# Kernel optimization log

Hardware: AMD Instinct MI355X
Metric: run time of the kernel (lower is better)

The kernel has to match this reference:

```python
import jax, jax.numpy as jnp
import numpy as np

B, N, NH = 16, 2048, 64
DROP = 0.1


def setup_inputs() -> dict:
    key = jax.random.key(0)
    ks = jax.random.split(key, 10)
    s = 1.0 / np.sqrt(NH)
    return {
        "adj": jax.random.normal(ks[0], (B, N, N), jnp.float32) * 0.02,
        "diff": jax.random.normal(ks[1], (B, N, N), jnp.float32) * 0.02,
        "sub_local_pos1": jax.random.normal(ks[2], (B, N, NH), jnp.float32),
        "sub_local_pos2": jax.random.normal(ks[3], (B, N, NH), jnp.float32),
        "sub_local_neg1": jax.random.normal(ks[4], (B, N, NH), jnp.float32),
        "sub_local_neg2": jax.random.normal(ks[5], (B, N, NH), jnp.float32),
        # Bilinear params: weight [1, NH, NH], bias [1] (xavier-ish scale)
        "W0": jax.random.normal(ks[6], (1, NH, NH), jnp.float32) * s,
        "b0": jnp.zeros((1,), jnp.float32),
        "W1": jax.random.normal(ks[7], (1, NH, NH), jnp.float32) * s,
        "b1": jnp.zeros((1,), jnp.float32),
        "W2": jax.random.normal(ks[8], (1, NH, NH), jnp.float32) * s,
        "b2": jnp.zeros((1,), jnp.float32),
        "alpha": jnp.full((1,), 0.5, jnp.float32),
        "beta": jnp.full((1,), 0.5, jnp.float32),
        "lamda": jnp.full((1,), 0.5, jnp.float32),
        "k": 0.5,  # static fraction kept per topk cascade
    }


def _bilinear(x, y, W, b):
    # nn.Bilinear(NH, NH, 1): out[b,n] = x[b,n,:] @ W[0] @ y[b,n,:] + b[0]
    return jnp.einsum('bni,ij,bnj->bn', x, W[0], y) + b[0]


def _select(X, idx):
    # Select module: sort indices along batch dim 0, then per-row gather
    idx = jnp.sort(idx, axis=0)
    return jnp.take_along_axis(X, idx[:, :, None], axis=1)


def _topk_idx(logits, k_frac):
    half = logits.shape[1] // 2
    score = jax.nn.sigmoid(logits[:, half:] - logits[:, :half])  # neg - pos
    _, idx_pos = jax.lax.top_k(score, half)
    return idx_pos[:, : int(k_frac * half)]


def _forward(adj, diff, pos1, pos2, neg1, neg2,
             W0, b0, W1, b1, W2, b2, alpha, beta, lamda, k):
    mkey = jax.random.key(1)
    m1 = jax.random.uniform(jax.random.fold_in(mkey, 0), (N, NH)) < DROP
    m2 = jax.random.uniform(jax.random.fold_in(mkey, 1), (N, NH)) < DROP
    p1 = jnp.where(m1, 0.0, pos1); n1 = jnp.where(m1, 0.0, neg1)
    p2 = jnp.where(m2, 0.0, pos2); n2 = jnp.where(m2, 0.0, neg2)

    fus_pos = (p1 + p2) * 0.5
    fus_neg = (n1 + n2) * 0.5

    # Readout = mean over node dim, then sigmoid, broadcast back to [B,N,NH]
    g1 = jnp.broadcast_to(jax.nn.sigmoid(jnp.mean(p1, axis=1))[:, None, :], p1.shape)
    g2 = jnp.broadcast_to(jax.nn.sigmoid(jnp.mean(p2, axis=1))[:, None, :], p2.shape)

    lf1 = jnp.concatenate([_bilinear(fus_pos, g1, W0, b0), _bilinear(fus_neg, g1, W0, b0)], 1)
    lf2 = jnp.concatenate([_bilinear(fus_pos, g2, W0, b0), _bilinear(fus_neg, g2, W0, b0)], 1)
    logits_fusion = alpha * lf1 + (1.0 - alpha) * lf2  # [B, 2N]

    idx = _topk_idx(logits_fusion, k)  # [B, K1]

    sel_pos = _select(fus_pos, idx)
    sel_neg = _select(fus_neg, idx)
    l1 = _select(jax.nn.sigmoid(jnp.einsum('bnm,bmh->bnh', adj, p1)), idx)
    l2 = _select(jax.nn.sigmoid(jnp.einsum('bnm,bmh->bnh', diff, p2)), idx)

    ls1 = jnp.concatenate([_bilinear(sel_pos, l1, W1, b1), _bilinear(sel_neg, l1, W1, b1)], 1)
    ls2 = jnp.concatenate([_bilinear(sel_pos, l2, W1, b1), _bilinear(sel_neg, l2, W1, b1)], 1)
    logits_fusion_sub = beta * ls1 + (1.0 - beta) * ls2  # [B, 2*K1]

    idx_sub = _topk_idx(logits_fusion_sub, k)  # [B, K2]

    sel_pos_sub = _select(sel_pos, idx_sub)
    sel_neg_sub = _select(sel_neg, idx_sub)
    l1s = _select(_select(jax.nn.sigmoid(p1), idx), idx_sub)
    l2s = _select(_select(jax.nn.sigmoid(p2), idx), idx_sub)

    lss1 = jnp.concatenate([_bilinear(sel_pos_sub, l1s, W2, b2), _bilinear(sel_neg_sub, l1s, W2, b2)], 1)
    lss2 = jnp.concatenate([_bilinear(sel_pos_sub, l2s, W2, b2), _bilinear(sel_neg_sub, l2s, W2, b2)], 1)
    logits_fusion_sub_sub = lamda * lss1 + (1.0 - lamda) * lss2  # [B, 2*K2]

    return (logits_fusion, logits_fusion_sub, logits_fusion_sub_sub)


def reference(adj, diff, sub_local_pos1, sub_local_pos2, sub_local_neg1, sub_local_neg2,
              W0, b0, W1, b1, W2, b2, alpha, beta, lamda, k):
    return _forward(adj, diff, sub_local_pos1, sub_local_pos2, sub_local_neg1, sub_local_neg2,
                    W0, b0, W1, b1, W2, b2, alpha, beta, lamda, k)
```

## Files before the change

kernel.cpp:

```cpp
#include <hip/hip_runtime.h>
#include <cstdint>
#include <cstddef>

static constexpr int Bn  = 16;
static constexpr int Nn  = 2048;
static constexpr int NHn = 64;
static constexpr int K1  = 1024;
static constexpr int K2  = 512;

__host__ __device__ inline void tf2x32(uint32_t k0, uint32_t k1, uint32_t& x0, uint32_t& x1) {
  const uint32_t ks0 = k0, ks1 = k1, ks2 = k0 ^ k1 ^ 0x1BD11BDAu;
  x0 += ks0; x1 += ks1;
  const int R[20] = {13,15,26,6, 17,29,16,24, 13,15,26,6, 17,29,16,24, 13,15,26,6};
  const uint32_t ks[3] = {ks0, ks1, ks2};
  int inj = 0;
  for (int r = 0; r < 20; ++r) {
    x0 += x1;
    x1 = (x1 << R[r]) | (x1 >> (32 - R[r]));
    x1 ^= x0;
    if ((r & 3) == 3) {
      ++inj;
      x0 += ks[inj % 3];
      x1 += ks[(inj + 1) % 3] + (uint32_t)inj;
    }
  }
}

__device__ __forceinline__ float xla_expf(float x) {
  const float LOG2EF   = 1.44269504088896341f;
  const float ln2_hi   = 0.693359375f;
  const float nln2_lo  = 2.12194440e-4f;
  const float p0 = 1.9875691500e-4f, p1c = 1.3981999507e-3f, p2c = 8.3334519073e-3f,
              p3c = 4.1665795894e-2f, p4c = 1.6666665459e-1f, p5c = 5.0000001201e-1f;
  float xc = fminf(fmaxf(x, -87.33654785f), 88.72283935f);
  float m = floorf(__fmaf_rn(xc, LOG2EF, 0.5f));
  float r = __fmaf_rn(m, -ln2_hi, xc);
  r = __fmaf_rn(m, nln2_lo, r);
  float r2 = __fmul_rn(r, r);
  float y = p0;
  y = __fmaf_rn(y, r, p1c);
  y = __fmaf_rn(y, r, p2c);
  y = __fmaf_rn(y, r, p3c);
  y = __fmaf_rn(y, r, p4c);
  y = __fmaf_rn(y, r, p5c);
  y = __fmaf_rn(y, r2, r);
  y = __fadd_rn(y, 1.0f);
  int n = (int)m;
  float s2 = __uint_as_float((uint32_t)(n + 127) << 23);
  return __fmul_rn(y, s2);
}

__device__ __forceinline__ float sigmoid_exp(float x) {
  float e = xla_expf(-x);
  return __fdiv_rn(1.0f, __fadd_rn(1.0f, e));
}

__device__ __forceinline__ unsigned long long pack_key(float s, int idx) {
  return ((unsigned long long)(__float_as_uint(s) ^ 0xFFFFFFFFu) << 32) | (uint32_t)idx;
}

__global__ void mask_kernel(uint32_t fk0a, uint32_t fk1a, uint32_t fk0b, uint32_t fk1b,
                            float* __restrict__ mask1, float* __restrict__ mask2) {
  int i = blockIdx.x * blockDim.x + threadIdx.x;
  if (i >= Nn * NHn) return;
  uint32_t x0 = 0u, x1 = (uint32_t)i;
  tf2x32(fk0a, fk1a, x0, x1);
  uint32_t bits = x0 ^ x1;
  float u = __uint_as_float((bits >> 9) | 0x3f800000u) - 1.0f;
  mask1[i] = (u < 0.1f) ? 1.0f : 0.0f;
  x0 = 0u; x1 = (uint32_t)i;
  tf2x32(fk0b, fk1b, x0, x1);
  bits = x0 ^ x1;
  u = __uint_as_float((bits >> 9) | 0x3f800000u) - 1.0f;
  mask2[i] = (u < 0.1f) ? 1.0f : 0.0f;
}

__global__ void drop_kernel(const float4* __restrict__ pos1, const float4* __restrict__ pos2,
                            const float4* __restrict__ mask1, const float4* __restrict__ mask2,
                            float4* __restrict__ p1, float4* __restrict__ p2) {
  size_t i4 = (size_t)blockIdx.x * blockDim.x + threadIdx.x;
  int nh4 = (int)(i4 & (size_t)(Nn * NHn / 4 - 1));
  float4 m1 = mask1[nh4], m2 = mask2[nh4];
  float4 a = pos1[i4], c = pos2[i4];
  float4 o1, o2;
  o1.x = (m1.x != 0.0f) ? 0.0f : a.x;  o1.y = (m1.y != 0.0f) ? 0.0f : a.y;
  o1.z = (m1.z != 0.0f) ? 0.0f : a.z;  o1.w = (m1.w != 0.0f) ? 0.0f : a.w;
  o2.x = (m2.x != 0.0f) ? 0.0f : c.x;  o2.y = (m2.y != 0.0f) ? 0.0f : c.y;
  o2.z = (m2.z != 0.0f) ? 0.0f : c.z;  o2.w = (m2.w != 0.0f) ? 0.0f : c.w;
  p1[i4] = o1;
  p2[i4] = o2;
}

__global__ void gmean_kernel(const float* __restrict__ p1, const float* __restrict__ p2,
                             float* __restrict__ g1, float* __restrict__ g2) {
  int b = blockIdx.x, h = threadIdx.x;
  const float* P1 = p1 + (size_t)b * Nn * NHn + h;
  const float* P2 = p2 + (size_t)b * Nn * NHn + h;
  float a1 = 0.0f, a2 = 0.0f;
  for (int n = 0; n < Nn; n += 8) {
    float v1[8], v2[8];
#pragma unroll
    for (int u = 0; u < 8; ++u) {
      v1[u] = P1[(size_t)(n + u) * NHn];
      v2[u] = P2[(size_t)(n + u) * NHn];
    }
#pragma unroll
    for (int u = 0; u < 8; ++u) {
      a1 = __fadd_rn(a1, v1[u]);
      a2 = __fadd_rn(a2, v2[u]);
    }
  }
  float m1 = __fdiv_rn(a1, 2048.0f);
  float m2 = __fdiv_rn(a2, 2048.0f);
  g1[b * 64 + h] = sigmoid_exp(m1);
  g2[b * 64 + h] = sigmoid_exp(m2);
}

__global__ __launch_bounds__(256) void logits1_np(
    const float* __restrict__ p1, const float* __restrict__ p2,
    const float* __restrict__ neg1, const float* __restrict__ neg2,
    const float* __restrict__ mask1, const float* __restrict__ mask2,
    const float* __restrict__ g1, const float* __restrict__ g2,
    const float* __restrict__ W0, const float* __restrict__ b0p,
    const float* __restrict__ alphap,
    float* __restrict__ out0, unsigned long long* __restrict__ key1) {
  __shared__ __align__(16) float xp[64][68], xn[64][68], w[4096], g[2][64];
  int b = blockIdx.y, n0 = blockIdx.x * 64, t = threadIdx.x;
  for (int c = 0; c < 16; ++c) {
    int idx = c * 256 + t, row = idx >> 6, i = idx & 63;
    size_t ga = ((size_t)b * Nn + n0 + row) * NHn + i;
    int ma = (n0 + row) * NHn + i;
    xp[row][i] = __fmul_rn(__fadd_rn(p1[ga], p2[ga]), 0.5f);
    float nv1 = (mask1[ma] != 0.0f) ? 0.0f : neg1[ga];
    float nv2 = (mask2[ma] != 0.0f) ? 0.0f : neg2[ga];
    xn[row][i] = __fmul_rn(__fadd_rn(nv1, nv2), 0.5f);
    w[idx] = W0[idx];
  }
  if (t < 64) { g[0][t] = g1[b * 64 + t]; g[1][t] = g2[b * 64 + t]; }
  __syncthreads();
  int row = t >> 2, e = t & 3;
  const float* x = (e & 2) ? &xn[row][0] : &xp[row][0];
  const float* gg = g[e & 1];
  float T[64];
#pragma unroll
  for (int j = 0; j < 64; ++j) T[j] = 0.0f;
  for (int i = 0; i < 64; ++i) {
    float xv = x[i];
#pragma unroll
    for (int jb = 0; jb < 16; ++jb) {
      float4 wv = *(const float4*)&w[i * 64 + jb * 4];
      T[jb * 4 + 0] = __fmaf_rn(xv, wv.x, T[jb * 4 + 0]);
      T[jb * 4 + 1] = __fmaf_rn(xv, wv.y, T[jb * 4 + 1]);
      T[jb * 4 + 2] = __fmaf_rn(xv, wv.z, T[jb * 4 + 2]);
      T[jb * 4 + 3] = __fmaf_rn(xv, wv.w, T[jb * 4 + 3]);
    }
  }
  float acc = 0.0f;
#pragma unroll
  for (int jb = 0; jb < 16; ++jb) {
    float4 gv = *(const float4*)&gg[jb * 4];
    acc = __fadd_rn(acc, __fmul_rn(T[jb * 4 + 0], gv.x));
    acc = __fadd_rn(acc, __fmul_rn(T[jb * 4 + 1], gv.y));
    acc = __fadd_rn(acc, __fmul_rn(T[jb * 4 + 2], gv.z));
    acc = __fadd_rn(acc, __fmul_rn(T[jb * 4 + 3], gv.w));
  }
  float a = __fadd_rn(acc, *b0p);
  float al = *alphap, om = __fsub_rn(1.0f, al);
  float other = __shfl_xor(a, 1);
  float L = __fadd_rn(__fmul_rn(al, a), __fmul_rn(om, other));
  float Lneg = __shfl_xor(L, 2);
  int n = n0 + row;
  if (e == 0) {
    out0[(size_t)b * (2 * Nn) + n] = L;
    float d = __fsub_rn(Lneg, L);
    key1[(size_t)b * Nn + n] = pack_key(sigmoid_exp(d), n);
  } else if (e == 2) {
    out0[(size_t)b * (2 * Nn) + Nn + n] = L;
  }
}

template <int S>
__global__ void topk_bitonic(const unsigned long long* __restrict__ keysrc,
                             int* __restrict__ idx_out) {
  constexpr int K = S / 2;
  __shared__ unsigned long long keys[S];
  int b = blockIdx.x;
  for (int i = threadIdx.x; i < S; i += blockDim.x)
    keys[i] = keysrc[(size_t)b * S + i];
  for (int k = 2; k <= S; k <<= 1) {
    for (int j = k >> 1; j > 0; j >>= 1) {
      __syncthreads();
      for (int t = threadIdx.x; t < S / 2; t += blockDim.x) {
        int i = ((t / j) * (j << 1)) + (t % j);
        unsigned long long a = keys[i], c = keys[i + j];
        if (((i & k) == 0) == (a > c)) { keys[i] = c; keys[i + j] = a; }
      }
    }
  }
  __syncthreads();
  for (int t = threadIdx.x; t < K; t += blockDim.x)
    idx_out[(size_t)b * K + t] = (int)(keys[t] & 0xffffffffu);
}

__global__ void colsort_kernel(const int* __restrict__ idx, int* __restrict__ sidx, int K) {
  int j = blockIdx.x * blockDim.x + threadIdx.x;
  if (j >= K) return;
  int v[16];
  for (int b = 0; b < 16; ++b) v[b] = idx[b * K + j];
  for (int a = 1; a < 16; ++a) {
    int x = v[a]; int c = a - 1;
    while (c >= 0 && v[c] > x) { v[c + 1] = v[c]; --c; }
    v[c + 1] = x;
  }
  for (int b = 0; b < 16; ++b) sidx[b * K + j] = v[b];
}

__global__ __launch_bounds__(256) void selmm_np7(const float* __restrict__ M0,
                                                 const float* __restrict__ M1,
                                                 const float* __restrict__ P0,
                                                 const float* __restrict__ P1,
                                                 const int* __restrict__ sidx,
                                                 float* __restrict__ L0,
                                                 float* __restrict__ L1) {
  __shared__ __align__(16) float ash[32][68];
  __shared__ __align__(16) float psh[64][64];
  __shared__ int rj[32];
  int b = blockIdx.y, j0 = blockIdx.x * 32, t = threadIdx.x;
  const float* M = blockIdx.z ? M1 : M0;
  const float* P = blockIdx.z ? P1 : P0;
  float* L = blockIdx.z ? L1 : L0;
  if (t < 32) rj[t] = sidx[b * K1 + j0 + t];
  __syncthreads();
  int cg = t & 15, rg = t >> 4;
  int r0 = rg * 2, r1 = r0 + 1;
  const float* Mb = M + (size_t)b * Nn * Nn;
  const float* Pb = P + (size_t)b * Nn * NHn;
  float acc00 = 0.f, acc01 = 0.f, acc02 = 0.f, acc03 = 0.f;
  float acc10 = 0.f, acc11 = 0.f, acc12 = 0.f, acc13 = 0.f;
  for (int m0 = 0; m0 < Nn; m0 += 64) {
#pragma unroll
    for (int pass = 0; pass < 2; ++pass) {
      int f = pass * 256 + t;
      int row = f >> 4, c4 = f & 15;
      *(float4*)&ash[row][c4 * 4] = *(const float4*)&Mb[(size_t)rj[row] * Nn + m0 + c4 * 4];
    }
#pragma unroll
    for (int pass = 0; pass < 4; ++pass) {
      int f = pass * 256 + t;
      int mm = f >> 4, c4 = f & 15;
      *(float4*)&psh[mm][c4 * 4] = *(const float4*)&Pb[(size_t)(m0 + mm) * NHn + c4 * 4];
    }
    __syncthreads();
#pragma unroll 4
    for (int mb = 0; mb < 16; ++mb) {
      float4 a0 = *(const float4*)&ash[r0][mb * 4];
      float4 a1 = *(const float4*)&ash[r1][mb * 4];
      float4 pv0 = *(const float4*)&psh[mb * 4 + 0][cg * 4];
      float4 pv1 = *(const float4*)&psh[mb * 4 + 1][cg * 4];
      float4 pv2 = *(const float4*)&psh[mb * 4 + 2][cg * 4];
      float4 pv3 = *(const float4*)&psh[mb * 4 + 3][cg * 4];
      acc00 = __fmaf_rn(a0.x, pv0.x, acc00);
      acc01 = __fmaf_rn(a0.x, pv0.y, acc01);
      acc02 = __fmaf_rn(a0.x, pv0.z, acc02);
      acc03 = __fmaf_rn(a0.x, pv0.w, acc03);
      acc10 = __fmaf_rn(a1.x, pv0.x, acc10);
      acc11 = __fmaf_rn(a1.x, pv0.y, acc11);
      acc12 = __fmaf_rn(a1.x, pv0.z, acc12);
      acc13 = __fmaf_rn(a1.x, pv0.w, acc13);
      acc00 = __fmaf_rn(a0.y, pv1.x, acc00);
      acc01 = __fmaf_rn(a0.y, pv1.y, acc01);
      acc02 = __fmaf_rn(a0.y, pv1.z, acc02);
      acc03 = __fmaf_rn(a0.y, pv1.w, acc03);
      acc10 = __fmaf_rn(a1.y, pv1.x, acc10);
      acc11 = __fmaf_rn(a1.y, pv1.y, acc11);
      acc12 = __fmaf_rn(a1.y, pv1.z, acc12);
      acc13 = __fmaf_rn(a1.y, pv1.w, acc13);
      acc00 = __fmaf_rn(a0.z, pv2.x, acc00);
      acc01 = __fmaf_rn(a0.z, pv2.y, acc01);
      acc02 = __fmaf_rn(a0.z, pv2.z, acc02);
      acc03 = __fmaf_rn(a0.z, pv2.w, acc03);
      acc10 = __fmaf_rn(a1.z, pv2.x, acc10);
      acc11 = __fmaf_rn(a1.z, pv2.y, acc11);
      acc12 = __fmaf_rn(a1.z, pv2.z, acc12);
      acc13 = __fmaf_rn(a1.z, pv2.w, acc13);
      acc00 = __fmaf_rn(a0.w, pv3.x, acc00);
      acc01 = __fmaf_rn(a0.w, pv3.y, acc01);
      acc02 = __fmaf_rn(a0.w, pv3.z, acc02);
      acc03 = __fmaf_rn(a0.w, pv3.w, acc03);
      acc10 = __fmaf_rn(a1.w, pv3.x, acc10);
      acc11 = __fmaf_rn(a1.w, pv3.y, acc11);
      acc12 = __fmaf_rn(a1.w, pv3.z, acc12);
      acc13 = __fmaf_rn(a1.w, pv3.w, acc13);
    }
    __syncthreads();
  }
  size_t base0 = ((size_t)b * K1 + j0 + r0) * NHn + cg * 4;
  size_t base1 = ((size_t)b * K1 + j0 + r1) * NHn + cg * 4;
  L[base0 + 0] = sigmoid_exp(acc00);
  L[base0 + 1] = sigmoid_exp(acc01);
  L[base0 + 2] = sigmoid_exp(acc02);
  L[base0 + 3] = sigmoid_exp(acc03);
  L[base1 + 0] = sigmoid_exp(acc10);
  L[base1 + 1] = sigmoid_exp(acc11);
  L[base1 + 2] = sigmoid_exp(acc12);
  L[base1 + 3] = sigmoid_exp(acc13);
}

__global__ __launch_bounds__(256) void logits2_np(
    const float* __restrict__ p1, const float* __restrict__ p2,
    const float* __restrict__ neg1, const float* __restrict__ neg2,
    const float* __restrict__ mask1, const float* __restrict__ mask2,
    const int* __restrict__ sidx1,
    const float* __restrict__ l1, const float* __restrict__ l2,
    const float* __restrict__ W1, const float* __restrict__ b1p,
    const float* __restrict__ betap,
    float* __restrict__ out1, unsigned long long* __restrict__ key2) {
  __shared__ __align__(16) float xp[64][68], xn[64][68], y1s[64][68], y2s[64][68], w[4096];
  __shared__ int rrs[64];
  int b = blockIdx.y, j0 = blockIdx.x * 64, t = threadIdx.x;
  if (t < 64) rrs[t] = sidx1[b * K1 + j0 + t];
  __syncthreads();
  for (int c = 0; c < 16; ++c) {
    int idx = c * 256 + t, row = idx >> 6, i = idx & 63;
    int rr = rrs[row];
    size_t ga = ((size_t)b * Nn + rr) * NHn + i;
    int ma = rr * NHn + i;
    xp[row][i] = __fmul_rn(__fadd_rn(p1[ga], p2[ga]), 0.5f);
    float nv1 = (mask1[ma] != 0.0f) ? 0.0f : neg1[ga];
    float nv2 = (mask2[ma] != 0.0f) ? 0.0f : neg2[ga];
    xn[row][i] = __fmul_rn(__fadd_rn(nv1, nv2), 0.5f);
    size_t la = ((size_t)b * K1 + j0 + row) * NHn + i;
    y1s[row][i] = l1[la];
    y2s[row][i] = l2[la];
    w[idx] = W1[idx];
  }
  __syncthreads();
  int row = t >> 2, e = t & 3;
  const float* x = (e & 2) ? &xn[row][0] : &xp[row][0];
  const float* yy = (e & 1) ? &y2s[row][0] : &y1s[row][0];
  float T[64];
#pragma unroll
  for (int j = 0; j < 64; ++j) T[j] = 0.0f;
  for (int i = 0; i < 64; ++i) {
    float xv = x[i];
#pragma unroll
    for (int jb = 0; jb < 16; ++jb) {
      float4 wv = *(const float4*)&w[i * 64 + jb * 4];
      T[jb * 4 + 0] = __fmaf_rn(xv, wv.x, T[jb * 4 + 0]);
      T[jb * 4 + 1] = __fmaf_rn(xv, wv.y, T[jb * 4 + 1]);
      T[jb * 4 + 2] = __fmaf_rn(xv, wv.z, T[jb * 4 + 2]);
      T[jb * 4 + 3] = __fmaf_rn(xv, wv.w, T[jb * 4 + 3]);
    }
  }
  float acc = 0.0f;
#pragma unroll
  for (int jb = 0; jb < 16; ++jb) {
    float4 yv = *(const float4*)&yy[jb * 4];
    acc = __fadd_rn(acc, __fmul_rn(T[jb * 4 + 0], yv.x));
    acc = __fadd_rn(acc, __fmul_rn(T[jb * 4 + 1], yv.y));
    acc = __fadd_rn(acc, __fmul_rn(T[jb * 4 + 2], yv.z));
    acc = __fadd_rn(acc, __fmul_rn(T[jb * 4 + 3], yv.w));
  }
  float a = __fadd_rn(acc, *b1p);
  float be = *betap, om = __fsub_rn(1.0f, be);
  float other = __shfl_xor(a, 1);
  float L = __fadd_rn(__fmul_rn(be, a), __fmul_rn(om, other));
  float Lneg = __shfl_xor(L, 2);
  int j = j0 + row;
  if (e == 0) {
    out1[(size_t)b * (2 * K1) + j] = L;
    float d = __fsub_rn(Lneg, L);
    key2[(size_t)b * K1 + j] = pack_key(sigmoid_exp(d), j);
  } else if (e == 2) {
    out1[(size_t)b * (2 * K1) + K1 + j] = L;
  }
}

__global__ void logits3_kernel(const float* __restrict__ p1, const float* __restrict__ p2,
                               const float* __restrict__ neg1, const float* __restrict__ neg2,
                               const float* __restrict__ mask1, const float* __restrict__ mask2,
                               const int* __restrict__ sidx1, const int* __restrict__ sidx2,
                               const float* __restrict__ W2,
                               const float* __restrict__ b2p, const float* __restrict__ lamp,
                               float* __restrict__ out2) {
  int b = blockIdx.y, tt = blockIdx.x, h = threadIdx.x;
  int rr = sidx1[b * K1 + sidx2[b * K2 + tt]];
  __shared__ float XP[64], XN[64];
  size_t xb = ((size_t)b * Nn + rr) * NHn + h;
  int ma = rr * NHn + h;
  float pv1 = p1[xb], pv2 = p2[xb];
  float nv1 = (mask1[ma] != 0.0f) ? 0.0f : neg1[xb];
  float nv2 = (mask2[ma] != 0.0f) ? 0.0f : neg2[xb];
  XP[h] = (pv1 + pv2) * 0.5f;
  XN[h] = (nv1 + nv2) * 0.5f;
  __syncthreads();
  float tp = 0.f, tn = 0.f;
#pragma unroll 8
  for (int i = 0; i < 64; ++i) {
    float ww = W2[i * 64 + h];
    tp = fmaf(XP[i], ww, tp);
    tn = fmaf(XN[i], ww, tn);
  }
  float y1 = sigmoid_exp(pv1);
  float y2 = sigmoid_exp(pv2);
  float p11 = tp * y1, p12 = tp * y2, p21 = tn * y1, p22 = tn * y2;
  for (int o = 32; o > 0; o >>= 1) {
    p11 += __shfl_down(p11, o);
    p12 += __shfl_down(p12, o);
    p21 += __shfl_down(p21, o);
    p22 += __shfl_down(p22, o);
  }
  if (h == 0) {
    float bb = *b2p, lm = *lamp;
    out2[(size_t)b * (2 * K2) + tt]      = lm * (p11 + bb) + (1.0f - lm) * (p12 + bb);
    out2[(size_t)b * (2 * K2) + K2 + tt] = lm * (p21 + bb) + (1.0f - lm) * (p22 + bb);
  }
}

extern "C" void kernel_launch(void* const* d_in, const int* in_sizes, int n_in,
                              void* d_out, int out_size, void* d_ws, size_t ws_size,
                              hipStream_t stream) {
  (void)in_sizes; (void)n_in; (void)out_size; (void)ws_size;

  const float* adj   = (const float*)d_in[0];
  const float* diff  = (const float*)d_in[1];
  const float* pos1  = (const float*)d_in[2];
  const float* pos2  = (const float*)d_in[3];
  const float* neg1  = (const float*)d_in[4];
  const float* neg2  = (const float*)d_in[5];
  const float* W0    = (const float*)d_in[6];
  const float* b0    = (const float*)d_in[7];
  const float* W1    = (const float*)d_in[8];
  const float* b1    = (const float*)d_in[9];
  const float* W2    = (const float*)d_in[10];
  const float* b2    = (const float*)d_in[11];
  const float* alpha = (const float*)d_in[12];
  const float* beta  = (const float*)d_in[13];
  const float* lamda = (const float*)d_in[14];

  float* out0 = (float*)d_out;
  float* out1 = out0 + Bn * 2 * Nn;
  float* out2 = out1 + Bn * 2 * K1;

  char* w = (char*)d_ws;
  size_t off = 0;
  auto alloc = [&](size_t bytes) -> void* {
    void* p = w + off;
    off += (bytes + 255) & ~(size_t)255;
    return p;
  };
  float* mask1 = (float*)alloc((size_t)Nn * NHn * 4);
  float* mask2 = (float*)alloc((size_t)Nn * NHn * 4);
  float* p1    = (float*)alloc((size_t)Bn * Nn * NHn * 4);
  float* p2    = (float*)alloc((size_t)Bn * Nn * NHn * 4);
  float* g1    = (float*)alloc((size_t)Bn * 64 * 4);
  float* g2    = (float*)alloc((size_t)Bn * 64 * 4);
  unsigned long long* key1 = (unsigned long long*)alloc((size_t)Bn * Nn * 8);
  unsigned long long* key2 = (unsigned long long*)alloc((size_t)Bn * K1 * 8);
  int*   idx1  = (int*)alloc((size_t)Bn * K1 * 4);
  int*   sidx1 = (int*)alloc((size_t)Bn * K1 * 4);
  int*   idx2  = (int*)alloc((size_t)Bn * K2 * 4);
  int*   sidx2 = (int*)alloc((size_t)Bn * K2 * 4);
  float* l1    = (float*)alloc((size_t)Bn * K1 * NHn * 4);
  float* l2    = (float*)alloc((size_t)Bn * K1 * NHn * 4);

  uint32_t fk0a = 0u, fk1a = 0u;
  { uint32_t x0 = 0u, x1 = 0u; tf2x32(0u, 1u, x0, x1); fk0a = x0; fk1a = x1; }
  uint32_t fk0b = 0u, fk1b = 0u;
  { uint32_t x0 = 0u, x1 = 1u; tf2x32(0u, 1u, x0, x1); fk0b = x0; fk1b = x1; }

  mask_kernel<<<(Nn * NHn + 255) / 256, 256, 0, stream>>>(fk0a, fk1a, fk0b, fk1b, mask1, mask2);

  drop_kernel<<<(Bn * Nn * NHn / 4) / 256, 256, 0, stream>>>(
      (const float4*)pos1, (const float4*)pos2, (const float4*)mask1, (const float4*)mask2,
      (float4*)p1, (float4*)p2);

  gmean_kernel<<<Bn, 64, 0, stream>>>(p1, p2, g1, g2);

  logits1_np<<<dim3(Nn / 64, Bn), 256, 0, stream>>>(p1, p2, neg1, neg2, mask1, mask2,
                                                    g1, g2, W0, b0, alpha, out0, key1);

  topk_bitonic<2048><<<Bn, 1024, 0, stream>>>(key1, idx1);
  colsort_kernel<<<K1 / 256, 256, 0, stream>>>(idx1, sidx1, K1);

  selmm_np7<<<dim3(K1 / 32, Bn, 2), 256, 0, stream>>>(adj, diff, p1, p2, sidx1, l1, l2);

  logits2_np<<<dim3(K1 / 64, Bn), 256, 0, stream>>>(p1, p2, neg1, neg2, mask1, mask2,
                                                    sidx1, l1, l2, W1, b1, beta, out1, key2);

  topk_bitonic<1024><<<Bn, 512, 0, stream>>>(key2, idx2);
  colsort_kernel<<<K2 / 256, 256, 0, stream>>>(idx2, sidx2, K2);

  logits3_kernel<<<dim3(K2, Bn), 64, 0, stream>>>(p1, p2, neg1, neg2, mask1, mask2,
                                                  sidx1, sidx2, W2, b2, lamda, out2);
}
```

Baseline: 331.5 us.

## Register-prefetch next tile in selmm and use 4x4 register blocking with 128 threads

```diff
diff --git a/kernel.cpp b/kernel.cpp
--- a/kernel.cpp
+++ b/kernel.cpp
@@ -215,7 +215,7 @@
   for (int b = 0; b < 16; ++b) sidx[b * K + j] = v[b];
 }
 
-__global__ __launch_bounds__(256) void selmm_np7(const float* __restrict__ M0,
+__global__ __launch_bounds__(128) void selmm_np9(const float* __restrict__ M0,
                                                  const float* __restrict__ M1,
                                                  const float* __restrict__ P0,
                                                  const float* __restrict__ P1,
@@ -232,78 +232,72 @@
   if (t < 32) rj[t] = sidx[b * K1 + j0 + t];
   __syncthreads();
   int cg = t & 15, rg = t >> 4;
-  int r0 = rg * 2, r1 = r0 + 1;
+  int r0 = rg * 4;
   const float* Mb = M + (size_t)b * Nn * Nn;
   const float* Pb = P + (size_t)b * Nn * NHn;
-  float acc00 = 0.f, acc01 = 0.f, acc02 = 0.f, acc03 = 0.f;
-  float acc10 = 0.f, acc11 = 0.f, acc12 = 0.f, acc13 = 0.f;
+  int s_c4 = t & 15, s_r = t >> 4;
+  int arow[4];
+#pragma unroll
+  for (int q = 0; q < 4; ++q) arow[q] = rj[s_r + q * 8];
+  float4 ra[4], rp[8];
+#pragma unroll
+  for (int q = 0; q < 4; ++q)
+    ra[q] = *(const float4*)&Mb[(size_t)arow[q] * Nn + 0 + s_c4 * 4];
+#pragma unroll
+  for (int q = 0; q < 8; ++q)
+    rp[q] = *(const float4*)&Pb[(size_t)(0 + s_r + q * 8) * NHn + s_c4 * 4];
+
+  float acc[4][4];
+#pragma unroll
+  for (int r = 0; r < 4; ++r)
+#pragma unroll
+    for (int c = 0; c < 4; ++c) acc[r][c] = 0.0f;
+
   for (int m0 = 0; m0 < Nn; m0 += 64) {
 #pragma unroll
-    for (int pass = 0; pass < 2; ++pass) {
-      int f = pass * 256 + t;
-      int row = f >> 4, c4 = f & 15;
-      *(float4*)&ash[row][c4 * 4] = *(const float4*)&Mb[(size_t)rj[row] * Nn + m0 + c4 * 4];
-    }
-#pragma unroll
-    for (int pass = 0; pass < 4; ++pass) {
-      int f = pass * 256 + t;
-      int mm = f >> 4, c4 = f & 15;
-      *(float4*)&psh[mm][c4 * 4] = *(const float4*)&Pb[(size_t)(m0 + mm) * NHn + c4 * 4];
-    }
+    for (int q = 0; q < 4; ++q) *(float4*)&ash[s_r + q * 8][s_c4 * 4] = ra[q];
+#pragma unroll
+    for (int q = 0; q < 8; ++q) *(float4*)&psh[s_r + q * 8][s_c4 * 4] = rp[q];
     __syncthreads();
+    int mn = m0 + 64;
+    if (mn < Nn) {
+#pragma unroll
+      for (int q = 0; q < 4; ++q)
+        ra[q] = *(const float4*)&Mb[(size_t)arow[q] * Nn + mn + s_c4 * 4];
+#pragma unroll
+      for (int q = 0; q < 8; ++q)
+        rp[q] = *(const float4*)&Pb[(size_t)(mn + s_r + q * 8) * NHn + s_c4 * 4];
+    }
 #pragma unroll 4
     for (int mb = 0; mb < 16; ++mb) {
-      float4 a0 = *(const float4*)&ash[r0][mb * 4];
-      float4 a1 = *(const float4*)&ash[r1][mb * 4];
-      float4 pv0 = *(const float4*)&psh[mb * 4 + 0][cg * 4];
-      float4 pv1 = *(const float4*)&psh[mb * 4 + 1][cg * 4];
-      float4 pv2 = *(const float4*)&psh[mb * 4 + 2][cg * 4];
-      float4 pv3 = *(const float4*)&psh[mb * 4 + 3][cg * 4];
-      acc00 = __fmaf_rn(a0.x, pv0.x, acc00);
-      acc01 = __fmaf_rn(a0.x, pv0.y, acc01);
-      acc02 = __fmaf_rn(a0.x, pv0.z, acc02);
-      acc03 = __fmaf_rn(a0.x, pv0.w, acc03);
-      acc10 = __fmaf_rn(a1.x, pv0.x, acc10);
-      acc11 = __fmaf_rn(a1.x, pv0.y, acc11);
-      acc12 = __fmaf_rn(a1.x, pv0.z, acc12);
-      acc13 = __fmaf_rn(a1.x, pv0.w, acc13);
-      acc00 = __fmaf_rn(a0.y, pv1.x, acc00);
-      acc01 = __fmaf_rn(a0.y, pv1.y, acc01);
-      acc02 = __fmaf_rn(a0.y, pv1.z, acc02);
-      acc03 = __fmaf_rn(a0.y, pv1.w, acc03);
-      acc10 = __fmaf_rn(a1.y, pv1.x, acc10);
-      acc11 = __fmaf_rn(a1.y, pv1.y, acc11);
-      acc12 = __fmaf_rn(a1.y, pv1.z, acc12);
-      acc13 = __fmaf_rn(a1.y, pv1.w, acc13);
-      acc00 = __fmaf_rn(a0.z, pv2.x, acc00);
-      acc01 = __fmaf_rn(a0.z, pv2.y, acc01);
-      acc02 = __fmaf_rn(a0.z, pv2.z, acc02);
-      acc03 = __fmaf_rn(a0.z, pv2.w, acc03);
-      acc10 = __fmaf_rn(a1.z, pv2.x, acc10);
-      acc11 = __fmaf_rn(a1.z, pv2.y, acc11);
-      acc12 = __fmaf_rn(a1.z, pv2.z, acc12);
-      acc13 = __fmaf_rn(a1.z, pv2.w, acc13);
-      acc00 = __fmaf_rn(a0.w, pv3.x, acc00);
-      acc01 = __fmaf_rn(a0.w, pv3.y, acc01);
-      acc02 = __fmaf_rn(a0.w, pv3.z, acc02);
-      acc03 = __fmaf_rn(a0.w, pv3.w, acc03);
-      acc10 = __fmaf_rn(a1.w, pv3.x, acc10);
-      acc11 = __fmaf_rn(a1.w, pv3.y, acc11);
-      acc12 = __fmaf_rn(a1.w, pv3.z, acc12);
-      acc13 = __fmaf_rn(a1.w, pv3.w, acc13);
+      float4 av[4];
+#pragma unroll
+      for (int r = 0; r < 4; ++r) av[r] = *(const float4*)&ash[r0 + r][mb * 4];
+      float4 pv[4];
+#pragma unroll
+      for (int q = 0; q < 4; ++q) pv[q] = *(const float4*)&psh[mb * 4 + q][cg * 4];
+#pragma unroll
+      for (int q = 0; q < 4; ++q) {
+#pragma unroll
+        for (int r = 0; r < 4; ++r) {
+          float am = (q == 0) ? av[r].x : (q == 1) ? av[r].y : (q == 2) ? av[r].z : av[r].w;
+          acc[r][0] = __fmaf_rn(am, pv[q].x, acc[r][0]);
+          acc[r][1] = __fmaf_rn(am, pv[q].y, acc[r][1]);
+          acc[r][2] = __fmaf_rn(am, pv[q].z, acc[r][2]);
+          acc[r][3] = __fmaf_rn(am, pv[q].w, acc[r][3]);
+        }
+      }
     }
     __syncthreads();
   }
-  size_t base0 = ((size_t)b * K1 + j0 + r0) * NHn + cg * 4;
-  size_t base1 = ((size_t)b * K1 + j0 + r1) * NHn + cg * 4;
-  L[base0 + 0] = sigmoid_exp(acc00);
-  L[base0 + 1] = sigmoid_exp(acc01);
-  L[base0 + 2] = sigmoid_exp(acc02);
-  L[base0 + 3] = sigmoid_exp(acc03);
-  L[base1 + 0] = sigmoid_exp(acc10);
-  L[base1 + 1] = sigmoid_exp(acc11);
-  L[base1 + 2] = sigmoid_exp(acc12);
-  L[base1 + 3] = sigmoid_exp(acc13);
+#pragma unroll
+  for (int r = 0; r < 4; ++r) {
+    size_t base = ((size_t)b * K1 + j0 + r0 + r) * NHn + cg * 4;
+    L[base + 0] = sigmoid_exp(acc[r][0]);
+    L[base + 1] = sigmoid_exp(acc[r][1]);
+    L[base + 2] = sigmoid_exp(acc[r][2]);
+    L[base + 3] = sigmoid_exp(acc[r][3]);
+  }
 }
 
 __global__ __launch_bounds__(256) void logits2_np(
@@ -483,7 +477,7 @@
   topk_bitonic<2048><<<Bn, 1024, 0, stream>>>(key1, idx1);
   colsort_kernel<<<K1 / 256, 256, 0, stream>>>(idx1, sidx1, K1);
 
-  selmm_np7<<<dim3(K1 / 32, Bn, 2), 256, 0, stream>>>(adj, diff, p1, p2, sidx1, l1, l2);
+  selmm_np9<<<dim3(K1 / 32, Bn, 2), 128, 0, stream>>>(adj, diff, p1, p2, sidx1, l1, l2);
 
   logits2_np<<<dim3(K1 / 64, Bn), 256, 0, stream>>>(p1, p2, neg1, neg2, mask1, mask2,
                                                     sidx1, l1, l2, W1, b1, beta, out1, key2);
```

Result: slower. 501.0 us (+51.1%).
